# Kernel optimization log

Measured on AMD Instinct MI355X. Metric: run time of the kernel, lower is better.

Reference implementation:

```python
import jax, jax.numpy as jnp
import numpy as np

D_MODEL = 1024
NUM_HEADS = 16
HEAD_DIM = D_MODEL // NUM_HEADS


def setup_inputs() -> dict:
    key = jax.random.key(0)
    ks = jax.random.split(key, 11)
    B, S = 4, 2048
    scale = 1.0 / np.sqrt(D_MODEL)
    inp = {
        "k": jax.random.normal(ks[0], (B, S, D_MODEL), jnp.float32),
        "q": jax.random.normal(ks[1], (B, S, D_MODEL), jnp.float32),
        "v": jax.random.normal(ks[2], (B, S, D_MODEL), jnp.float32),
        "w_k": jax.random.normal(ks[3], (D_MODEL, D_MODEL), jnp.float32) * scale,
        "b_k": jnp.zeros((D_MODEL,), jnp.float32),
        "w_q": jax.random.normal(ks[4], (D_MODEL, D_MODEL), jnp.float32) * scale,
        "b_q": jnp.zeros((D_MODEL,), jnp.float32),
        "w_v": jax.random.normal(ks[5], (D_MODEL, D_MODEL), jnp.float32) * scale,
        "b_v": jnp.zeros((D_MODEL,), jnp.float32),
        "w_o": jax.random.normal(ks[6], (D_MODEL, D_MODEL), jnp.float32) * scale,
        "b_o": jnp.zeros((D_MODEL,), jnp.float32),
    }
    return inp


def _split_heads(x):
    B, S, _ = x.shape
    return x.reshape(B, S, NUM_HEADS, HEAD_DIM).transpose(0, 2, 1, 3)  # [B,H,S,Dh]


def reference(k, q, v, w_k, b_k, w_q, b_q, w_v, b_v, w_o, b_o):
    # Linear projections (torch Linear: x @ W.T + b; here weights stored as [in,out])
    kp = k @ w_k + b_k
    qp = q @ w_q + b_q
    vp = v @ w_v + b_v
    kh = _split_heads(kp)
    qh = _split_heads(qp)
    vh = _split_heads(vp)
    # NOTE: original divides by head_dim, not sqrt(head_dim)
    scores = jnp.einsum("bhsd,bhtd->bhst", qh, kh) / HEAD_DIM
    attn = jax.nn.softmax(scores, axis=-1)
    # dropout is identity in eval mode (deterministic baseline)
    ctx = jnp.einsum("bhst,bhtd->bhsd", attn, vh)
    B, H, S, Dh = ctx.shape
    ctx = ctx.transpose(0, 2, 1, 3).reshape(B, S, D_MODEL)
    return ctx @ w_o + b_o
```

## Files before the change

### kernel.cpp

```cpp
#include <hip/hip_runtime.h>

#define D_MODEL 1024
#define S_LEN   2048
#define BATCH   4
#define NHEAD   16
#define HDIM    64
#define NTOK    (BATCH * S_LEN)

typedef __attribute__((ext_vector_type(8))) __bf16 bf16x8;
typedef __attribute__((ext_vector_type(4))) float  floatx4;

static __device__ inline floatx4 mfma16(bf16x8 a, bf16x8 b, floatx4 c) {
    return __builtin_amdgcn_mfma_f32_16x16x32_bf16(a, b, c, 0, 0, 0);
}

static __device__ inline void gload_lds16(const __bf16* g, __bf16* l) {
    __builtin_amdgcn_global_load_lds(
        (const __attribute__((address_space(1))) void*)g,
        (__attribute__((address_space(3))) void*)l, 16, 0, 0);
}

#define BARRIER()  asm volatile("s_barrier" ::: "memory")
#define WAITVM4()  asm volatile("s_waitcnt vmcnt(4)" ::: "memory")
#define WAITLGKM() asm volatile("s_waitcnt lgkmcnt(0)" ::: "memory")

#if __has_builtin(__builtin_amdgcn_exp2f)
#define EXP2(x) __builtin_amdgcn_exp2f(x)
#else
#define EXP2(x) exp2f(x)
#endif

static __device__ inline unsigned pack_bf16(float a, float b) {
    unsigned ua = __builtin_bit_cast(unsigned, a) + 0x8000u;
    unsigned ub = __builtin_bit_cast(unsigned, b) + 0x8000u;
#if __has_builtin(__builtin_amdgcn_perm)
    return __builtin_amdgcn_perm(ub, ua, 0x07060302u);
#else
    return (ua >> 16) | (ub & 0xffff0000u);
#endif
}

__global__ __launch_bounds__(256) void cvt_qkv(const float* __restrict__ k,
                                               const float* __restrict__ q,
                                               const float* __restrict__ v,
                                               __bf16* __restrict__ kb,
                                               __bf16* __restrict__ qb,
                                               __bf16* __restrict__ vb) {
    const float* x = (blockIdx.y == 0) ? k : (blockIdx.y == 1) ? q : v;
    __bf16* y = (blockIdx.y == 0) ? kb : (blockIdx.y == 1) ? qb : vb;
    size_t i = ((size_t)blockIdx.x * 256 + threadIdx.x) * 8;
    float4 a = *(const float4*)(x + i);
    float4 b = *(const float4*)(x + i + 4);
    bf16x8 o;
    o[0] = (__bf16)a.x; o[1] = (__bf16)a.y; o[2] = (__bf16)a.z; o[3] = (__bf16)a.w;
    o[4] = (__bf16)b.x; o[5] = (__bf16)b.y; o[6] = (__bf16)b.z; o[7] = (__bf16)b.w;
    *(bf16x8*)(y + i) = o;
}

__global__ __launch_bounds__(256) void cvt_w4(const float* __restrict__ w0,
                                              const float* __restrict__ w1,
                                              const float* __restrict__ w2,
                                              const float* __restrict__ w3,
                                              __bf16* __restrict__ t0,
                                              __bf16* __restrict__ t1,
                                              __bf16* __restrict__ t2,
                                              __bf16* __restrict__ t3) {
    const int z = blockIdx.z;
    const float* W = (z == 0) ? w0 : (z == 1) ? w1 : (z == 2) ? w2 : w3;
    __bf16* Wt = (z == 0) ? t0 : (z == 1) ? t1 : (z == 2) ? t2 : t3;
    __shared__ __bf16 t[64][72];
    const int i0 = blockIdx.x * 64;
    const int j0 = blockIdx.y * 64;
    const int tid = threadIdx.x;
    const int r4 = tid >> 4, c4 = (tid & 15) * 4;
#pragma unroll
    for (int rr = 0; rr < 64; rr += 16) {
        int r = rr + r4;
        float4 v = *(const float4*)(W + (size_t)(i0 + r) * D_MODEL + j0 + c4);
        t[c4 + 0][r] = (__bf16)v.x;
        t[c4 + 1][r] = (__bf16)v.y;
        t[c4 + 2][r] = (__bf16)v.z;
        t[c4 + 3][r] = (__bf16)v.w;
    }
    __syncthreads();
    const int r8 = tid >> 3, c8 = (tid & 7) * 8;
#pragma unroll
    for (int rr = 0; rr < 64; rr += 32) {
        int r = rr + r8;
        bf16x8 o;
#pragma unroll
        for (int e = 0; e < 8; e++) o[e] = t[r][c8 + e];
        *(bf16x8*)(Wt + (size_t)(j0 + r) * D_MODEL + i0 + c8) = o;
    }
}

#define BM 128
#define BN 128
#define BK 32
template <int OUT_F32>
__device__ __forceinline__ void gemm_body(const __bf16* __restrict__ A,
                                          const __bf16* __restrict__ Bt,
                                          void* __restrict__ Cp,
                                          const float* __restrict__ biasN,
                                          const float* __restrict__ biasM,
                                          int N, int K, float scale,
                                          int bm, int bn,
                                          __bf16* lA, __bf16* lB) {
    const int tid = threadIdx.x;
    const int wave = tid >> 6, lane = tid & 63;
    const int quad = lane >> 4, l16 = lane & 15;
    const int wm = (wave >> 1) * 64, wn = (wave & 1) * 64;
    const int c0 = wave * 128 + lane;

    floatx4 acc[4][4];
#pragma unroll
    for (int i = 0; i < 4; i++)
#pragma unroll
        for (int j = 0; j < 4; j++) acc[i][j] = (floatx4){0.f, 0.f, 0.f, 0.f};

    const __bf16* Ag = A + (size_t)bm * K;
    const __bf16* Bg = Bt + (size_t)bn * K;

    for (int k0 = 0; k0 < K; k0 += BK) {
        __syncthreads();
#pragma unroll
        for (int i = 0; i < 2; i++) {
            int c = c0 + i * 64;
            int row = c >> 2, col = (c & 3) * 8;
            gload_lds16(Ag + (size_t)row * K + k0 + col, lA + c * 8);
            gload_lds16(Bg + (size_t)row * K + k0 + col, lB + c * 8);
        }
        __syncthreads();
        bf16x8 af[4], bf[4];
#pragma unroll
        for (int i = 0; i < 4; i++) {
            af[i] = *(const bf16x8*)(lA + (wm + i * 16 + l16) * BK + quad * 8);
            bf[i] = *(const bf16x8*)(lB + (wn + i * 16 + l16) * BK + quad * 8);
        }
#pragma unroll
        for (int i = 0; i < 4; i++)
#pragma unroll
            for (int j = 0; j < 4; j++) acc[i][j] = mfma16(af[i], bf[j], acc[i][j]);
    }

#pragma unroll
    for (int i = 0; i < 4; i++) {
#pragma unroll
        for (int r = 0; r < 4; r++) {
            int row = bm + wm + i * 16 + quad * 4 + r;
            float brow = biasM ? biasM[row] : 0.0f;
#pragma unroll
            for (int j = 0; j < 4; j++) {
                int col = bn + wn + j * 16 + l16;
                float v = (acc[i][j][r] + brow + (biasN ? biasN[col] : 0.0f)) * scale;
                if constexpr (OUT_F32)
                    ((float*)Cp)[(size_t)row * N + col] = v;
                else
                    ((__bf16*)Cp)[(size_t)row * N + col] = (__bf16)v;
            }
        }
    }
}

__global__ __launch_bounds__(256) void qkv_gemm(const __bf16* __restrict__ kb,
                                                const __bf16* __restrict__ qb,
                                                const __bf16* __restrict__ vb,
                                                const __bf16* __restrict__ WtK,
                                                const __bf16* __restrict__ WtQ,
                                                const __bf16* __restrict__ WtV,
                                                __bf16* Kp, __bf16* Qp, __bf16* Vtp,
                                                const float* b_k, const float* b_q,
                                                const float* b_v, float qscale) {
    __shared__ __bf16 lA[BM * BK];
    __shared__ __bf16 lB[BN * BK];
    const int z = blockIdx.z;
    if (z == 0)
        gemm_body<0>(kb, WtK, Kp, b_k, nullptr, D_MODEL, D_MODEL, 1.0f,
                     blockIdx.x * BM, blockIdx.y * BN, lA, lB);
    else if (z == 1)
        gemm_body<0>(qb, WtQ, Qp, b_q, nullptr, D_MODEL, D_MODEL, qscale,
                     blockIdx.x * BM, blockIdx.y * BN, lA, lB);
    else
        gemm_body<0>(WtV, vb, Vtp, nullptr, b_v, NTOK, D_MODEL, 1.0f,
                     blockIdx.y * BM, blockIdx.x * BN, lA, lB);
}

__global__ __launch_bounds__(256) void out_gemm(const __bf16* __restrict__ A,
                                                const __bf16* __restrict__ Bt,
                                                float* __restrict__ C,
                                                const float* __restrict__ biasN) {
    __shared__ __bf16 lA[BM * BK];
    __shared__ __bf16 lB[BN * BK];
    gemm_body<1>(A, Bt, C, biasN, nullptr, D_MODEL, D_MODEL, 1.0f,
                 blockIdx.x * BM, blockIdx.y * BN, lA, lB);
}

#define QT_M 256
#define KVT  64

template <int CUR>
__device__ __forceinline__ void attn_step(
    __bf16 (&lK)[2][KVT * HDIM], __bf16 (&lV)[2][HDIM * KVT], __bf16* lPw,
    const __bf16* Kg, const __bf16* Vg, int t0n,
    const bf16x8 (&qf)[4][2], floatx4 (&octx)[4][4], float (&lsum)[4],
    int tid, int quad, int l16, int swz) {
    constexpr int NXT = CUR ^ 1;

    BARRIER();
#pragma unroll
    for (int i = 0; i < 2; i++) {
        int g = i * 256 + tid;
        int row = g >> 3, cl = (g & 7) ^ (row & 7);
        gload_lds16(Kg + (size_t)(t0n + row) * D_MODEL + cl * 8, &lK[NXT][g * 8]);
        gload_lds16(Vg + (size_t)row * NTOK + t0n + cl * 8, &lV[NXT][g * 8]);
    }
    WAITVM4();
    BARRIER();

#pragma unroll
    for (int tt = 0; tt < 4; tt++) {
        bf16x8 kf0 = *(const bf16x8*)(&lK[CUR][(tt * 16 + l16) * HDIM + ((0 + quad) ^ swz) * 8]);
        bf16x8 kf1 = *(const bf16x8*)(&lK[CUR][(tt * 16 + l16) * HDIM + ((4 + quad) ^ swz) * 8]);
        floatx4 sc[4];
#pragma unroll
        for (int m = 0; m < 4; m++) {
            sc[m] = mfma16(kf0, qf[m][0], (floatx4){0.f, 0.f, 0.f, 0.f});
            sc[m] = mfma16(kf1, qf[m][1], sc[m]);
        }
        int c = tt * 4 + quad;
        int g = c >> 1, half = c & 1;
        int off = ((g ^ swz) * 8 + half * 4);
#pragma unroll
        for (int m = 0; m < 4; m++) {
            float p0 = EXP2(sc[m][0]), p1 = EXP2(sc[m][1]);
            float p2 = EXP2(sc[m][2]), p3 = EXP2(sc[m][3]);
            lsum[m] += (p0 + p1) + (p2 + p3);
            unsigned lo = pack_bf16(p0, p1), hi = pack_bf16(p2, p3);
            *(uint2*)(lPw + (m * 16 + l16) * 64 + off) = make_uint2(lo, hi);
        }
    }
    WAITLGKM();

#pragma unroll
    for (int kh = 0; kh < 2; kh++) {
        int goff = (((kh << 2) | quad) ^ swz) * 8;
        bf16x8 vf[4], pf[4];
#pragma unroll
        for (int j = 0; j < 4; j++)
            vf[j] = *(const bf16x8*)(&lV[CUR][(j * 16 + l16) * KVT + goff]);
#pragma unroll
        for (int m = 0; m < 4; m++)
            pf[m] = *(const bf16x8*)(lPw + (m * 16 + l16) * 64 + goff);
#pragma unroll
        for (int m = 0; m < 4; m++)
#pragma unroll
            for (int j = 0; j < 4; j++)
                octx[m][j] = mfma16(pf[m], vf[j], octx[m][j]);
    }
}

__global__ __launch_bounds__(256, 2) void attn(const __bf16* __restrict__ Qp,
                                               const __bf16* __restrict__ Kp,
                                               const __bf16* __restrict__ Vt,
                                               __bf16* __restrict__ ctx) {
    const int qt = blockIdx.x, h = blockIdx.y, b = blockIdx.z;
    const int tid = threadIdx.x;
    const int wave = tid >> 6, lane = tid & 63;
    const int quad = lane >> 4, l16 = lane & 15;
    const int swz = l16 & 7;

    __shared__ __bf16 lK[2][KVT * HDIM];
    __shared__ __bf16 lV[2][HDIM * KVT];
    __shared__ __bf16 lP[4][64 * 64];

    const int qbase = b * S_LEN + qt * QT_M + wave * 64;
    bf16x8 qf[4][2];
#pragma unroll
    for (int m = 0; m < 4; m++)
#pragma unroll
        for (int hf = 0; hf < 2; hf++)
            qf[m][hf] = *(const bf16x8*)(Qp + (size_t)(qbase + m * 16 + l16) * D_MODEL +
                                         h * HDIM + hf * 32 + quad * 8);

    floatx4 octx[4][4];
    float lsum[4];
#pragma unroll
    for (int m = 0; m < 4; m++) {
#pragma unroll
        for (int j = 0; j < 4; j++) octx[m][j] = (floatx4){0.f, 0.f, 0.f, 0.f};
        lsum[m] = 0.f;
    }

    const __bf16* Kg = Kp + (size_t)(b * S_LEN) * D_MODEL + h * HDIM;
    const __bf16* Vg = Vt + (size_t)(h * HDIM) * NTOK + (size_t)b * S_LEN;

#pragma unroll
    for (int i = 0; i < 2; i++) {
        int g = i * 256 + tid;
        int row = g >> 3, cl = (g & 7) ^ (row & 7);
        gload_lds16(Kg + (size_t)row * D_MODEL + cl * 8, &lK[0][g * 8]);
        gload_lds16(Vg + (size_t)row * NTOK + cl * 8, &lV[0][g * 8]);
    }

    __bf16* lPw = &lP[wave][0];

    for (int it2 = 0; it2 < S_LEN / KVT / 2; ++it2) {
        attn_step<0>(lK, lV, lPw, Kg, Vg, (2 * it2 + 1) * KVT,
                     qf, octx, lsum, tid, quad, l16, swz);
        attn_step<1>(lK, lV, lPw, Kg, Vg, ((2 * it2 + 2) * KVT) & (S_LEN - 1),
                     qf, octx, lsum, tid, quad, l16, swz);
    }

#pragma unroll
    for (int m = 0; m < 4; m++) {
        float l = lsum[m];
        l += __shfl_xor(l, 16, 64);
        l += __shfl_xor(l, 32, 64);
#pragma unroll
        for (int r = 0; r < 4; r++) {
            float linv = 1.0f / __shfl(l, quad * 4 + r, 64);
            int qrow = qbase + m * 16 + quad * 4 + r;
#pragma unroll
            for (int j = 0; j < 4; j++) {
                int col = h * HDIM + j * 16 + l16;
                ctx[(size_t)qrow * D_MODEL + col] = (__bf16)(octx[m][j][r] * linv);
            }
        }
    }
}

extern "C" void kernel_launch(void* const* d_in, const int* in_sizes, int n_in,
                              void* d_out, int out_size, void* d_ws, size_t ws_size,
                              hipStream_t stream) {
    (void)in_sizes; (void)n_in; (void)out_size; (void)ws_size;
    const float* k_in = (const float*)d_in[0];
    const float* q_in = (const float*)d_in[1];
    const float* v_in = (const float*)d_in[2];
    const float* w_k  = (const float*)d_in[3];
    const float* b_k  = (const float*)d_in[4];
    const float* w_q  = (const float*)d_in[5];
    const float* b_q  = (const float*)d_in[6];
    const float* w_v  = (const float*)d_in[7];
    const float* b_v  = (const float*)d_in[8];
    const float* w_o  = (const float*)d_in[9];
    const float* b_o  = (const float*)d_in[10];

    char* ws = (char*)d_ws;
    const size_t SZ = (size_t)NTOK * D_MODEL * sizeof(__bf16);
    __bf16* kb  = (__bf16*)(ws + 0 * SZ);
    __bf16* qb  = (__bf16*)(ws + 1 * SZ);
    __bf16* vb  = (__bf16*)(ws + 2 * SZ);
    __bf16* WtK = (__bf16*)(ws + 3 * SZ);
    __bf16* WtQ = WtK + (size_t)D_MODEL * D_MODEL;
    __bf16* WtV = WtQ + (size_t)D_MODEL * D_MODEL;
    __bf16* WtO = WtV + (size_t)D_MODEL * D_MODEL;
    __bf16* Kp  = (__bf16*)(ws + 3 * SZ + 4 * (size_t)D_MODEL * D_MODEL * sizeof(__bf16));
    __bf16* Qp  = Kp + (size_t)NTOK * D_MODEL;
    __bf16* Vtp = Qp + (size_t)NTOK * D_MODEL;
    __bf16* ctx = kb;

    const float QSCALE = 1.44269504f / 64.0f;

    cvt_qkv<<<dim3(NTOK * D_MODEL / (256 * 8), 3), 256, 0, stream>>>(
        k_in, q_in, v_in, kb, qb, vb);
    cvt_w4<<<dim3(16, 16, 4), 256, 0, stream>>>(w_k, w_q, w_v, w_o, WtK, WtQ, WtV, WtO);

    qkv_gemm<<<dim3(64, 8, 3), 256, 0, stream>>>(kb, qb, vb, WtK, WtQ, WtV,
                                                 Kp, Qp, Vtp, b_k, b_q, b_v, QSCALE);

    attn<<<dim3(S_LEN / QT_M, NHEAD, BATCH), 256, 0, stream>>>(Qp, Kp, Vtp, ctx);

    out_gemm<<<dim3(64, 8), 256, 0, stream>>>(ctx, WtO, (float*)d_out, b_o);
}
```

Before: 358.2 us.

## Double GEMM K-tile with swizzled LDS and relax attention LDS waits

The projection GEMMs now load 64-wide K tiles through an XOR-swizzled LDS layout and run two MFMA sub-steps per tile. This halves the number of barrier pairs per K loop and is meant to avoid LDS bank conflicts. Their launch bounds now request three blocks per CU. In attention, the full lgkmcnt(0) wait before the PV stage becomes a partial lgkmcnt(8) wait at each K-half, so the first half of the P-times-V products can start while later P stores are still pending. The row-sum accumulator is also split into two partial sums to shorten the dependency chain. The larger tile doubles the LDS use per GEMM block, and the partial wait relies on LDS operations completing in issue order.

```diff
diff --git a/kernel.cpp b/kernel.cpp
--- a/kernel.cpp
+++ b/kernel.cpp
@@ -20,9 +20,9 @@
         (__attribute__((address_space(3))) void*)l, 16, 0, 0);
 }
 
-#define BARRIER()  asm volatile("s_barrier" ::: "memory")
-#define WAITVM4()  asm volatile("s_waitcnt vmcnt(4)" ::: "memory")
-#define WAITLGKM() asm volatile("s_waitcnt lgkmcnt(0)" ::: "memory")
+#define BARRIER()   asm volatile("s_barrier" ::: "memory")
+#define WAITVM4()   asm volatile("s_waitcnt vmcnt(4)" ::: "memory")
+#define WAITLGKM8() asm volatile("s_waitcnt lgkmcnt(8)" ::: "memory")
 
 #if __has_builtin(__builtin_amdgcn_exp2f)
 #define EXP2(x) __builtin_amdgcn_exp2f(x)
@@ -96,7 +96,7 @@
 
 #define BM 128
 #define BN 128
-#define BK 32
+#define BK 64
 template <int OUT_F32>
 __device__ __forceinline__ void gemm_body(const __bf16* __restrict__ A,
                                           const __bf16* __restrict__ Bt,
@@ -109,8 +109,8 @@
     const int tid = threadIdx.x;
     const int wave = tid >> 6, lane = tid & 63;
     const int quad = lane >> 4, l16 = lane & 15;
+    const int swz = l16 & 7;
     const int wm = (wave >> 1) * 64, wn = (wave & 1) * 64;
-    const int c0 = wave * 128 + lane;
 
     floatx4 acc[4][4];
 #pragma unroll
@@ -124,23 +124,27 @@
     for (int k0 = 0; k0 < K; k0 += BK) {
         __syncthreads();
 #pragma unroll
-        for (int i = 0; i < 2; i++) {
-            int c = c0 + i * 64;
-            int row = c >> 2, col = (c & 3) * 8;
-            gload_lds16(Ag + (size_t)row * K + k0 + col, lA + c * 8);
-            gload_lds16(Bg + (size_t)row * K + k0 + col, lB + c * 8);
+        for (int i = 0; i < 4; i++) {
+            int g = i * 256 + tid;
+            int row = g >> 3, cl = (g & 7) ^ (row & 7);
+            gload_lds16(Ag + (size_t)row * K + k0 + cl * 8, lA + g * 8);
+            gload_lds16(Bg + (size_t)row * K + k0 + cl * 8, lB + g * 8);
         }
         __syncthreads();
-        bf16x8 af[4], bf[4];
-#pragma unroll
-        for (int i = 0; i < 4; i++) {
-            af[i] = *(const bf16x8*)(lA + (wm + i * 16 + l16) * BK + quad * 8);
-            bf[i] = *(const bf16x8*)(lB + (wn + i * 16 + l16) * BK + quad * 8);
-        }
-#pragma unroll
-        for (int i = 0; i < 4; i++)
-#pragma unroll
-            for (int j = 0; j < 4; j++) acc[i][j] = mfma16(af[i], bf[j], acc[i][j]);
+#pragma unroll
+        for (int kk = 0; kk < 2; kk++) {
+            bf16x8 af[4], bf[4];
+#pragma unroll
+            for (int i = 0; i < 4; i++) {
+                int ra = wm + i * 16 + l16, rb = wn + i * 16 + l16;
+                af[i] = *(const bf16x8*)(lA + ra * BK + ((kk * 4 + quad) ^ swz) * 8);
+                bf[i] = *(const bf16x8*)(lB + rb * BK + ((kk * 4 + quad) ^ swz) * 8);
+            }
+#pragma unroll
+            for (int i = 0; i < 4; i++)
+#pragma unroll
+                for (int j = 0; j < 4; j++) acc[i][j] = mfma16(af[i], bf[j], acc[i][j]);
+        }
     }
 
 #pragma unroll
@@ -162,15 +166,15 @@
     }
 }
 
-__global__ __launch_bounds__(256) void qkv_gemm(const __bf16* __restrict__ kb,
-                                                const __bf16* __restrict__ qb,
-                                                const __bf16* __restrict__ vb,
-                                                const __bf16* __restrict__ WtK,
-                                                const __bf16* __restrict__ WtQ,
-                                                const __bf16* __restrict__ WtV,
-                                                __bf16* Kp, __bf16* Qp, __bf16* Vtp,
-                                                const float* b_k, const float* b_q,
-                                                const float* b_v, float qscale) {
+__global__ __launch_bounds__(256, 3) void qkv_gemm(const __bf16* __restrict__ kb,
+                                                   const __bf16* __restrict__ qb,
+                                                   const __bf16* __restrict__ vb,
+                                                   const __bf16* __restrict__ WtK,
+                                                   const __bf16* __restrict__ WtQ,
+                                                   const __bf16* __restrict__ WtV,
+                                                   __bf16* Kp, __bf16* Qp, __bf16* Vtp,
+                                                   const float* b_k, const float* b_q,
+                                                   const float* b_v, float qscale) {
     __shared__ __bf16 lA[BM * BK];
     __shared__ __bf16 lB[BN * BK];
     const int z = blockIdx.z;
@@ -185,10 +189,10 @@
                      blockIdx.y * BM, blockIdx.x * BN, lA, lB);
 }
 
-__global__ __launch_bounds__(256) void out_gemm(const __bf16* __restrict__ A,
-                                                const __bf16* __restrict__ Bt,
-                                                float* __restrict__ C,
-                                                const float* __restrict__ biasN) {
+__global__ __launch_bounds__(256, 3) void out_gemm(const __bf16* __restrict__ A,
+                                                   const __bf16* __restrict__ Bt,
+                                                   float* __restrict__ C,
+                                                   const float* __restrict__ biasN) {
     __shared__ __bf16 lA[BM * BK];
     __shared__ __bf16 lB[BN * BK];
     gemm_body<1>(A, Bt, C, biasN, nullptr, D_MODEL, D_MODEL, 1.0f,
@@ -202,7 +206,7 @@
 __device__ __forceinline__ void attn_step(
     __bf16 (&lK)[2][KVT * HDIM], __bf16 (&lV)[2][HDIM * KVT], __bf16* lPw,
     const __bf16* Kg, const __bf16* Vg, int t0n,
-    const bf16x8 (&qf)[4][2], floatx4 (&octx)[4][4], float (&lsum)[4],
+    const bf16x8 (&qf)[4][2], floatx4 (&octx)[4][4], float2 (&lsum2)[4],
     int tid, int quad, int l16, int swz) {
     constexpr int NXT = CUR ^ 1;
 
@@ -218,31 +222,36 @@
     BARRIER();
 
 #pragma unroll
-    for (int tt = 0; tt < 4; tt++) {
-        bf16x8 kf0 = *(const bf16x8*)(&lK[CUR][(tt * 16 + l16) * HDIM + ((0 + quad) ^ swz) * 8]);
-        bf16x8 kf1 = *(const bf16x8*)(&lK[CUR][(tt * 16 + l16) * HDIM + ((4 + quad) ^ swz) * 8]);
-        floatx4 sc[4];
-#pragma unroll
-        for (int m = 0; m < 4; m++) {
-            sc[m] = mfma16(kf0, qf[m][0], (floatx4){0.f, 0.f, 0.f, 0.f});
-            sc[m] = mfma16(kf1, qf[m][1], sc[m]);
-        }
-        int c = tt * 4 + quad;
-        int g = c >> 1, half = c & 1;
-        int off = ((g ^ swz) * 8 + half * 4);
-#pragma unroll
-        for (int m = 0; m < 4; m++) {
-            float p0 = EXP2(sc[m][0]), p1 = EXP2(sc[m][1]);
-            float p2 = EXP2(sc[m][2]), p3 = EXP2(sc[m][3]);
-            lsum[m] += (p0 + p1) + (p2 + p3);
-            unsigned lo = pack_bf16(p0, p1), hi = pack_bf16(p2, p3);
-            *(uint2*)(lPw + (m * 16 + l16) * 64 + off) = make_uint2(lo, hi);
-        }
-    }
-    WAITLGKM();
+    for (int half = 0; half < 2; half++) {
+#pragma unroll
+        for (int tt2 = 0; tt2 < 2; tt2++) {
+            const int tt = half * 2 + tt2;
+            bf16x8 kf0 = *(const bf16x8*)(&lK[CUR][(tt * 16 + l16) * HDIM + ((0 + quad) ^ swz) * 8]);
+            bf16x8 kf1 = *(const bf16x8*)(&lK[CUR][(tt * 16 + l16) * HDIM + ((4 + quad) ^ swz) * 8]);
+            floatx4 sc[4];
+#pragma unroll
+            for (int m = 0; m < 4; m++) {
+                sc[m] = mfma16(kf0, qf[m][0], (floatx4){0.f, 0.f, 0.f, 0.f});
+                sc[m] = mfma16(kf1, qf[m][1], sc[m]);
+            }
+            int c = tt * 4 + quad;
+            int g = c >> 1, hf = c & 1;
+            int off = ((g ^ swz) * 8 + hf * 4);
+#pragma unroll
+            for (int m = 0; m < 4; m++) {
+                float p0 = EXP2(sc[m][0]), p1 = EXP2(sc[m][1]);
+                float p2 = EXP2(sc[m][2]), p3 = EXP2(sc[m][3]);
+                lsum2[m].x += p0 + p1;
+                lsum2[m].y += p2 + p3;
+                unsigned lo = pack_bf16(p0, p1), hi = pack_bf16(p2, p3);
+                *(uint2*)(lPw + (m * 16 + l16) * 64 + off) = make_uint2(lo, hi);
+            }
+        }
+    }
 
 #pragma unroll
     for (int kh = 0; kh < 2; kh++) {
+        WAITLGKM8();
         int goff = (((kh << 2) | quad) ^ swz) * 8;
         bf16x8 vf[4], pf[4];
 #pragma unroll
@@ -283,12 +292,12 @@
                                          h * HDIM + hf * 32 + quad * 8);
 
     floatx4 octx[4][4];
-    float lsum[4];
+    float2 lsum2[4];
 #pragma unroll
     for (int m = 0; m < 4; m++) {
 #pragma unroll
         for (int j = 0; j < 4; j++) octx[m][j] = (floatx4){0.f, 0.f, 0.f, 0.f};
-        lsum[m] = 0.f;
+        lsum2[m] = make_float2(0.f, 0.f);
     }
 
     const __bf16* Kg = Kp + (size_t)(b * S_LEN) * D_MODEL + h * HDIM;
@@ -306,14 +315,14 @@
 
     for (int it2 = 0; it2 < S_LEN / KVT / 2; ++it2) {
         attn_step<0>(lK, lV, lPw, Kg, Vg, (2 * it2 + 1) * KVT,
-                     qf, octx, lsum, tid, quad, l16, swz);
+                     qf, octx, lsum2, tid, quad, l16, swz);
         attn_step<1>(lK, lV, lPw, Kg, Vg, ((2 * it2 + 2) * KVT) & (S_LEN - 1),
-                     qf, octx, lsum, tid, quad, l16, swz);
+                     qf, octx, lsum2, tid, quad, l16, swz);
     }
 
 #pragma unroll
     for (int m = 0; m < 4; m++) {
-        float l = lsum[m];
+        float l = lsum2[m].x + lsum2[m].y;
         l += __shfl_xor(l, 16, 64);
         l += __shfl_xor(l, 32, 64);
 #pragma unroll
```

Result: faster. 342.2 us (-4.5%).
